# Performance work log

Hardware: AMD Instinct MI355X
Metric: run time of the kernel (lower is better)

The kernel has to match this reference:

```python
import jax, jax.numpy as jnp
import numpy as np

LR_POS = 0.45   # adj_lr_pos: max(i/iters - 1, 0.45) == 0.45 always
LR_SIZE = 0.4
ITERS = 5
BOARD = 640.0


def box_iou(a, b):
    """Pairwise IoU. a: [..., N, 4], b: [..., M, 4] in pascal_voc -> [..., N, M]."""
    area_a = (a[..., 2] - a[..., 0]) * (a[..., 3] - a[..., 1])
    area_b = (b[..., 2] - b[..., 0]) * (b[..., 3] - b[..., 1])
    lt = jnp.maximum(a[..., :, None, :2], b[..., None, :, :2])
    rb = jnp.minimum(a[..., :, None, 2:], b[..., None, :, 2:])
    wh = jnp.clip(rb - lt, 0.0)
    inter = wh[..., 0] * wh[..., 1]
    union = area_a[..., :, None] + area_b[..., None, :] - inter
    return inter / union


def _make_boxes(key, shape, scale):
    # valid pascal_voc boxes: x1<x2, y1<y2
    corners = jax.random.uniform(key, shape[:-1] + (2, 2), dtype=jnp.float32)
    lo = jnp.min(corners, axis=-2)
    hi = jnp.max(corners, axis=-2) + 0.01  # avoid degenerate zero-area boxes
    return jnp.concatenate([lo, hi], axis=-1) * scale


def setup_inputs() -> dict:
    key = jax.random.key(0)
    k1, k2 = jax.random.split(key)
    B, N, M = 64, 1000, 100
    boxes = _make_boxes(k1, (B, N, 4), BOARD)
    gt_boxes = _make_boxes(k2, (B, M, 4), BOARD)
    return {"boxes": boxes, "gt_boxes": gt_boxes}


def reference(boxes, gt_boxes):
    """Batched progressive box adjustment toward best-IoU ground truth.

    boxes: [B, N, 4], gt_boxes: [B, M, 4], both pascal_voc.
    Returns (all_boxes [B, ITERS+1, N, 4], all_sims [B, ITERS+1, N, M]).
    """
    iou0 = box_iou(boxes, gt_boxes)  # [B, N, M]

    def step(carry, _):
        b, iou = carry
        best = jnp.argmax(iou, axis=-1)                                   # [B, N]
        best_gt = jnp.take_along_axis(gt_boxes, best[..., None], axis=1)  # [B, N, 4]
        cur_center = (b[..., :2] + b[..., 2:]) / 2
        gt_center = (best_gt[..., :2] + best_gt[..., 2:]) / 2
        delta_center = gt_center - cur_center
        delta_size = (best_gt[..., 2:] - best_gt[..., :2]) - (b[..., 2:] - b[..., :2])
        new_lt = b[..., :2] + LR_POS * delta_center
        new_rb = b[..., 2:] + LR_POS * delta_center + LR_SIZE * (delta_size - delta_center)
        new_b = jnp.concatenate([new_lt, new_rb], axis=-1)
        new_iou = box_iou(new_b, gt_boxes)
        return (new_b, new_iou), (new_b, new_iou)

    _, (boxes_seq, iou_seq) = jax.lax.scan(step, (boxes, iou0), None, length=ITERS)
    # prepend initial state: [ITERS+1, B, ...] -> [B, ITERS+1, ...]
    all_boxes = jnp.concatenate([boxes[None], boxes_seq], axis=0).transpose(1, 0, 2, 3)
    all_sims = jnp.concatenate([iou0[None], iou_seq], axis=0).transpose(1, 0, 2, 3)
    return all_boxes, all_sims
```

## Files before the change

### kernel.cpp

```cpp
#include <hip/hip_runtime.h>


#define BB 64
#define NN 1000
#define MM 100
#define NITER 5
#define RPW 16
#define MPL 25
#define SSTR 100

__global__ __launch_bounds__(256) void dvg_kernel(
    const float* __restrict__ boxes, const float* __restrict__ gt,
    float* __restrict__ out) {
  __shared__ float4 lgt[MM];
  __shared__ float lsims[4][RPW][SSTR];

  const int tid = threadIdx.x;
  const int wv = tid >> 6;
  const int lane = tid & 63;
  const int r = lane & 15;
  const int g = lane >> 4;
  const int b = blockIdx.x >> 4;
  const int n0 = (blockIdx.x & 15) * 64 + wv * RPW;
  const int n = n0 + r;
  const int nc = n < NN ? n : NN - 1;

  for (int i = tid; i < MM; i += 256)
    lgt[i] = reinterpret_cast<const float4*>(gt)[b * MM + i];
  __syncthreads();

  float areaG[MPL];
#pragma unroll
  for (int j = 0; j < MPL; ++j) {
    const float4 q = lgt[g * MPL + j];
    float a = (q.z - q.x) * (q.w - q.y);
    asm("" : "+v"(a));
    areaG[j] = a;
  }

  const float4 bx = reinterpret_cast<const float4*>(boxes)[b * NN + nc];
  float b0 = bx.x, b1 = bx.y, b2 = bx.z, b3 = bx.w;

  float* __restrict__ outB = out;
  float* __restrict__ outS = out + (size_t)BB * 6 * NN * 4;

  const int bp_addr = ((((lane & 3) << 4) + (lane >> 2)) << 2);
  const int rr = lane >> 2;
  const int q4 = (lane & 3) << 2;

  for (int it = 0;; ++it) {
    float area = (b2 - b0) * (b3 - b1);
    asm("" : "+v"(area));

    float v[MPL];
    float best = -1.0f;
    int bim = 0;
#pragma unroll
    for (int j = 0; j < MPL; ++j) {
      const float4 q = lgt[g * MPL + j];
      const float ltx = fmaxf(b0, q.x), lty = fmaxf(b1, q.y);
      const float rbx = fminf(b2, q.z), rby = fminf(b3, q.w);
      const float w = fmaxf(rbx - ltx, 0.0f);
      const float h = fmaxf(rby - lty, 0.0f);
      float inter = w * h;
      asm("" : "+v"(inter));
      const float uni = (area + areaG[j]) - inter;
      const float val = inter * __builtin_amdgcn_rcpf(uni);
      v[j] = val;
      const bool t = val > best;
      best = t ? val : best;
      bim = t ? g * MPL + j : bim;
    }

    {
      float* ls = &lsims[wv][r][g * MPL];
#pragma unroll
      for (int j = 0; j < MPL; ++j) ls[j] = v[j];
    }

    const size_t obase = (size_t)(b * 6 + it) * NN + n0;

    {
      const float t = g == 0 ? b0 : (g == 1 ? b1 : (g == 2 ? b2 : b3));
      const float bt = __int_as_float(
          __builtin_amdgcn_ds_bpermute(bp_addr, __float_as_int(t)));
      if (n0 + rr < NN) outB[obase * 4 + lane] = bt;
    }

    {
      const float* lsr = &lsims[wv][0][0];
      float* os = outS + obase * MM;
      const bool rowok = (n0 + rr) < NN;
#pragma unroll
      for (int i = 0; i < 7; ++i) {
        const int q = i * 4 + (lane & 3);
        if (q < MPL && rowok) {
          const float4 d =
              *reinterpret_cast<const float4*>(&lsr[rr * SSTR + i * 16 + q4]);
          *reinterpret_cast<float4*>(&os[(size_t)rr * MM + i * 16 + q4]) = d;
        }
      }
    }

    if (it == NITER) break;

#pragma unroll
    for (int off = 16; off <= 32; off <<= 1) {
      const float ov = __shfl_xor(best, off, 64);
      const int obi = __shfl_xor(bim, off, 64);
      const bool t = (ov > best) || (ov == best && obi < bim);
      best = t ? ov : best;
      bim = t ? obi : bim;
    }

    const float4 gg = lgt[bim];
    const float dcx = (gg.x + gg.z) * 0.5f - (b0 + b2) * 0.5f;
    const float dcy = (gg.y + gg.w) * 0.5f - (b1 + b3) * 0.5f;
    const float dsx = (gg.z - gg.x) - (b2 - b0);
    const float dsy = (gg.w - gg.y) - (b3 - b1);
    float px = 0.45f * dcx;
    asm("" : "+v"(px));
    float py = 0.45f * dcy;
    asm("" : "+v"(py));
    float qx = 0.4f * (dsx - dcx);
    asm("" : "+v"(qx));
    float qy = 0.4f * (dsy - dcy);
    asm("" : "+v"(qy));
    b0 = b0 + px;
    b1 = b1 + py;
    b2 = (b2 + px) + qx;
    b3 = (b3 + py) + qy;
  }
}

extern "C" void kernel_launch(void* const* d_in, const int* in_sizes, int n_in,
                              void* d_out, int out_size, void* d_ws,
                              size_t ws_size, hipStream_t stream) {
  const float* boxes = (const float*)d_in[0];
  const float* gt = (const float*)d_in[1];
  float* out = (float*)d_out;
  dvg_kernel<<<BB * 16, 256, 0, stream>>>(boxes, gt, out);
}
```

Measured before the change: 35.90 us.

## Remap lanes so each thread writes float4 IoU chunks directly, dropping LDS staging

```diff
diff --git a/kernel.cpp b/kernel.cpp
--- a/kernel.cpp
+++ b/kernel.cpp
@@ -5,38 +5,26 @@
 #define NN 1000
 #define MM 100
 #define NITER 5
-#define RPW 16
-#define MPL 25
-#define SSTR 100
 
-__global__ __launch_bounds__(256) void dvg_kernel(
+__global__ __launch_bounds__(128, 8) void dvg_kernel(
     const float* __restrict__ boxes, const float* __restrict__ gt,
     float* __restrict__ out) {
   __shared__ float4 lgt[MM];
-  __shared__ float lsims[4][RPW][SSTR];
 
   const int tid = threadIdx.x;
   const int wv = tid >> 6;
   const int lane = tid & 63;
-  const int r = lane & 15;
-  const int g = lane >> 4;
-  const int b = blockIdx.x >> 4;
-  const int n0 = (blockIdx.x & 15) * 64 + wv * RPW;
+  const int r = lane >> 2;
+  const int g = lane & 3;
+  const int b = blockIdx.x >> 5;
+  const int n0 = (blockIdx.x & 31) * 32 + wv * 16;
   const int n = n0 + r;
-  const int nc = n < NN ? n : NN - 1;
+  const bool vrow = n < NN;
+  const int nc = vrow ? n : NN - 1;
 
-  for (int i = tid; i < MM; i += 256)
+  for (int i = tid; i < MM; i += 128)
     lgt[i] = reinterpret_cast<const float4*>(gt)[b * MM + i];
   __syncthreads();
-
-  float areaG[MPL];
-#pragma unroll
-  for (int j = 0; j < MPL; ++j) {
-    const float4 q = lgt[g * MPL + j];
-    float a = (q.z - q.x) * (q.w - q.y);
-    asm("" : "+v"(a));
-    areaG[j] = a;
-  }
 
   const float4 bx = reinterpret_cast<const float4*>(boxes)[b * NN + nc];
   float b0 = bx.x, b1 = bx.y, b2 = bx.z, b3 = bx.w;
@@ -44,68 +32,50 @@
   float* __restrict__ outB = out;
   float* __restrict__ outS = out + (size_t)BB * 6 * NN * 4;
 
-  const int bp_addr = ((((lane & 3) << 4) + (lane >> 2)) << 2);
-  const int rr = lane >> 2;
-  const int q4 = (lane & 3) << 2;
+  for (int it = 0;; ++it) {
+    asm volatile("" ::: "memory");
 
-  for (int it = 0;; ++it) {
     float area = (b2 - b0) * (b3 - b1);
     asm("" : "+v"(area));
 
-    float v[MPL];
     float best = -1.0f;
     int bim = 0;
+    const size_t obase = (size_t)(b * 6 + it) * NN + n0;
+    float* __restrict__ os = outS + obase * MM + (size_t)r * MM;
+
 #pragma unroll
-    for (int j = 0; j < MPL; ++j) {
-      const float4 q = lgt[g * MPL + j];
-      const float ltx = fmaxf(b0, q.x), lty = fmaxf(b1, q.y);
-      const float rbx = fminf(b2, q.z), rby = fminf(b3, q.w);
-      const float w = fmaxf(rbx - ltx, 0.0f);
-      const float h = fmaxf(rby - lty, 0.0f);
-      float inter = w * h;
-      asm("" : "+v"(inter));
-      const float uni = (area + areaG[j]) - inter;
-      const float val = inter * __builtin_amdgcn_rcpf(uni);
-      v[j] = val;
-      const bool t = val > best;
-      best = t ? val : best;
-      bim = t ? g * MPL + j : bim;
-    }
-
-    {
-      float* ls = &lsims[wv][r][g * MPL];
+    for (int k = 0; k < 7; ++k) {
+      if (k < 6 || g == 0) {
+        float4 d;
 #pragma unroll
-      for (int j = 0; j < MPL; ++j) ls[j] = v[j];
-    }
-
-    const size_t obase = (size_t)(b * 6 + it) * NN + n0;
-
-    {
-      const float t = g == 0 ? b0 : (g == 1 ? b1 : (g == 2 ? b2 : b3));
-      const float bt = __int_as_float(
-          __builtin_amdgcn_ds_bpermute(bp_addr, __float_as_int(t)));
-      if (n0 + rr < NN) outB[obase * 4 + lane] = bt;
-    }
-
-    {
-      const float* lsr = &lsims[wv][0][0];
-      float* os = outS + obase * MM;
-      const bool rowok = (n0 + rr) < NN;
-#pragma unroll
-      for (int i = 0; i < 7; ++i) {
-        const int q = i * 4 + (lane & 3);
-        if (q < MPL && rowok) {
-          const float4 d =
-              *reinterpret_cast<const float4*>(&lsr[rr * SSTR + i * 16 + q4]);
-          *reinterpret_cast<float4*>(&os[(size_t)rr * MM + i * 16 + q4]) = d;
+        for (int c = 0; c < 4; ++c) {
+          const int m = 16 * k + 4 * g + c;
+          const float4 q = lgt[m];
+          float ag = (q.z - q.x) * (q.w - q.y);
+          asm("" : "+v"(ag));
+          const float w = fmaxf(fminf(b2, q.z) - fmaxf(b0, q.x), 0.0f);
+          const float h = fmaxf(fminf(b3, q.w) - fmaxf(b1, q.y), 0.0f);
+          float inter = w * h;
+          asm("" : "+v"(inter));
+          const float uni = (area + ag) - inter;
+          const float val = inter * __builtin_amdgcn_rcpf(uni);
+          (&d.x)[c] = val;
+          const bool t = val > best;
+          best = t ? val : best;
+          bim = t ? m : bim;
         }
+        if (vrow) *reinterpret_cast<float4*>(os + 16 * k + 4 * g) = d;
       }
     }
 
+    if (vrow) {
+      const float comp = g == 0 ? b0 : (g == 1 ? b1 : (g == 2 ? b2 : b3));
+      outB[obase * 4 + lane] = comp;
+    }
     if (it == NITER) break;
 
 #pragma unroll
-    for (int off = 16; off <= 32; off <<= 1) {
+    for (int off = 1; off <= 2; off <<= 1) {
       const float ov = __shfl_xor(best, off, 64);
       const int obi = __shfl_xor(bim, off, 64);
       const bool t = (ov > best) || (ov == best && obi < bim);
@@ -139,5 +109,5 @@
   const float* boxes = (const float*)d_in[0];
   const float* gt = (const float*)d_in[1];
   float* out = (float*)d_out;
-  dvg_kernel<<<BB * 16, 256, 0, stream>>>(boxes, gt, out);
+  dvg_kernel<<<BB * 32, 128, 0, stream>>>(boxes, gt, out);
 }
```

Measured after the change: 38.60 us. 7.5% more time.

## Split each box's GT scan across 8 lanes and double the grid

Applied to the files above, without the earlier changes.

```diff
diff --git a/kernel.cpp b/kernel.cpp
--- a/kernel.cpp
+++ b/kernel.cpp
@@ -5,11 +5,10 @@
 #define NN 1000
 #define MM 100
 #define NITER 5
-#define RPW 16
-#define MPL 25
-#define SSTR 100
+#define RPW 8
+#define SSTR 104
 
-__global__ __launch_bounds__(256) void dvg_kernel(
+__global__ __launch_bounds__(256, 8) void dvg_kernel(
     const float* __restrict__ boxes, const float* __restrict__ gt,
     float* __restrict__ out) {
   __shared__ float4 lgt[MM];
@@ -18,24 +17,29 @@
   const int tid = threadIdx.x;
   const int wv = tid >> 6;
   const int lane = tid & 63;
-  const int r = lane & 15;
-  const int g = lane >> 4;
-  const int b = blockIdx.x >> 4;
-  const int n0 = (blockIdx.x & 15) * 64 + wv * RPW;
-  const int n = n0 + r;
+  const int r = lane & 7;
+  const int g = lane >> 3;
+  const int b = blockIdx.x >> 5;
+  const int n0w = (blockIdx.x & 31) * 32 + wv * RPW;
+  const int n = n0w + r;
   const int nc = n < NN ? n : NN - 1;
+
+  const int LEN = g < 4 ? 13 : 12;
+  const int START = g < 4 ? 13 * g : 52 + 12 * (g - 4);
 
   for (int i = tid; i < MM; i += 256)
     lgt[i] = reinterpret_cast<const float4*>(gt)[b * MM + i];
   __syncthreads();
 
-  float areaG[MPL];
+  float areaG[13];
 #pragma unroll
-  for (int j = 0; j < MPL; ++j) {
-    const float4 q = lgt[g * MPL + j];
-    float a = (q.z - q.x) * (q.w - q.y);
-    asm("" : "+v"(a));
-    areaG[j] = a;
+  for (int j = 0; j < 13; ++j) {
+    if (j < LEN) {
+      const float4 q = lgt[START + j];
+      float a = (q.z - q.x) * (q.w - q.y);
+      asm("" : "+v"(a));
+      areaG[j] = a;
+    }
   }
 
   const float4 bx = reinterpret_cast<const float4*>(boxes)[b * NN + nc];
@@ -44,60 +48,59 @@
   float* __restrict__ outB = out;
   float* __restrict__ outS = out + (size_t)BB * 6 * NN * 4;
 
-  const int bp_addr = ((((lane & 3) << 4) + (lane >> 2)) << 2);
-  const int rr = lane >> 2;
-  const int q4 = (lane & 3) << 2;
+  const int bp_addr = (((lane >> 2) + ((lane & 3) << 3)) << 2);
+  const int rr = lane >> 3;
+  const int cq = lane & 7;
+  const bool rowok = (n0w + rr) < NN;
+  const bool boxok = lane < 32 && (n0w + (lane >> 2)) < NN;
 
   for (int it = 0;; ++it) {
     float area = (b2 - b0) * (b3 - b1);
     asm("" : "+v"(area));
 
-    float v[MPL];
     float best = -1.0f;
     int bim = 0;
+    {
+      float* ls = &lsims[wv][r][START];
 #pragma unroll
-    for (int j = 0; j < MPL; ++j) {
-      const float4 q = lgt[g * MPL + j];
-      const float ltx = fmaxf(b0, q.x), lty = fmaxf(b1, q.y);
-      const float rbx = fminf(b2, q.z), rby = fminf(b3, q.w);
-      const float w = fmaxf(rbx - ltx, 0.0f);
-      const float h = fmaxf(rby - lty, 0.0f);
-      float inter = w * h;
-      asm("" : "+v"(inter));
-      const float uni = (area + areaG[j]) - inter;
-      const float val = inter * __builtin_amdgcn_rcpf(uni);
-      v[j] = val;
-      const bool t = val > best;
-      best = t ? val : best;
-      bim = t ? g * MPL + j : bim;
+      for (int j = 0; j < 13; ++j) {
+        if (j < LEN) {
+          const float4 q = lgt[START + j];
+          const float ltx = fmaxf(b0, q.x), lty = fmaxf(b1, q.y);
+          const float rbx = fminf(b2, q.z), rby = fminf(b3, q.w);
+          const float w = fmaxf(rbx - ltx, 0.0f);
+          const float h = fmaxf(rby - lty, 0.0f);
+          float inter = w * h;
+          asm("" : "+v"(inter));
+          const float uni = (area + areaG[j]) - inter;
+          const float val = inter * __builtin_amdgcn_rcpf(uni);
+          ls[j] = val;
+          const bool t = val > best;
+          best = t ? val : best;
+          bim = t ? START + j : bim;
+        }
+      }
     }
 
-    {
-      float* ls = &lsims[wv][r][g * MPL];
-#pragma unroll
-      for (int j = 0; j < MPL; ++j) ls[j] = v[j];
-    }
+    const float tcomp = g == 0 ? b0 : (g == 1 ? b1 : (g == 2 ? b2 : b3));
+    const float bt = __int_as_float(
+        __builtin_amdgcn_ds_bpermute(bp_addr, __float_as_int(tcomp)));
 
-    const size_t obase = (size_t)(b * 6 + it) * NN + n0;
+    const size_t obase = (size_t)(b * 6 + it) * NN + n0w;
 
-    {
-      const float t = g == 0 ? b0 : (g == 1 ? b1 : (g == 2 ? b2 : b3));
-      const float bt = __int_as_float(
-          __builtin_amdgcn_ds_bpermute(bp_addr, __float_as_int(t)));
-      if (n0 + rr < NN) outB[obase * 4 + lane] = bt;
-    }
-
+    if (boxok) outB[obase * 4 + lane] = bt;
     {
       const float* lsr = &lsims[wv][0][0];
       float* os = outS + obase * MM;
-      const bool rowok = (n0 + rr) < NN;
 #pragma unroll
-      for (int i = 0; i < 7; ++i) {
-        const int q = i * 4 + (lane & 3);
-        if (q < MPL && rowok) {
-          const float4 d =
-              *reinterpret_cast<const float4*>(&lsr[rr * SSTR + i * 16 + q4]);
-          *reinterpret_cast<float4*>(&os[(size_t)rr * MM + i * 16 + q4]) = d;
+      for (int i = 0; i < 4; ++i) {
+        const int q = 8 * i + cq;
+        if (i < 3 || cq == 0) {
+          if (rowok) {
+            const float4 d =
+                *reinterpret_cast<const float4*>(&lsr[rr * SSTR + 4 * q]);
+            *reinterpret_cast<float4*>(&os[(size_t)rr * MM + 4 * q]) = d;
+          }
         }
       }
     }
@@ -105,7 +108,7 @@
     if (it == NITER) break;
 
 #pragma unroll
-    for (int off = 16; off <= 32; off <<= 1) {
+    for (int off = 8; off <= 32; off <<= 1) {
       const float ov = __shfl_xor(best, off, 64);
       const int obi = __shfl_xor(bim, off, 64);
       const bool t = (ov > best) || (ov == best && obi < bim);
@@ -139,5 +142,5 @@
   const float* boxes = (const float*)d_in[0];
   const float* gt = (const float*)d_in[1];
   float* out = (float*)d_out;
-  dvg_kernel<<<BB * 16, 256, 0, stream>>>(boxes, gt, out);
+  dvg_kernel<<<BB * 32, 256, 0, stream>>>(boxes, gt, out);
 }
```

Result: slower. 37.17 us (+3.5%).
